# Kernel optimization log

Hardware: AMD Instinct MI355X
Metric: run time of the kernel (lower is better)

Reference implementation:

```python
import jax, jax.numpy as jnp
import numpy as np

D_MODEL = 1024
NUM_HEADS = 16
D_K = D_MODEL // NUM_HEADS
B, S = 2, 2048


def setup_inputs() -> dict:
    key = jax.random.key(0)
    ks = jax.random.split(key, 11)
    sc = 1.0 / np.sqrt(D_MODEL)
    return {
        "Q_input": jax.random.normal(ks[0], (B, S, D_MODEL), jnp.float32),
        "K_input": jax.random.normal(ks[1], (B, S, D_MODEL), jnp.float32),
        "V_input": jax.random.normal(ks[2], (B, S, D_MODEL), jnp.float32),
        "Wq": jax.random.normal(ks[3], (D_MODEL, D_MODEL), jnp.float32) * sc,
        "bq": jax.random.normal(ks[4], (D_MODEL,), jnp.float32) * 0.01,
        "Wk": jax.random.normal(ks[5], (D_MODEL, D_MODEL), jnp.float32) * sc,
        "bk": jax.random.normal(ks[6], (D_MODEL,), jnp.float32) * 0.01,
        "Wv": jax.random.normal(ks[7], (D_MODEL, D_MODEL), jnp.float32) * sc,
        "bv": jax.random.normal(ks[8], (D_MODEL,), jnp.float32) * 0.01,
        "Wo": jax.random.normal(ks[9], (D_MODEL, D_MODEL), jnp.float32) * sc,
        "bo": jax.random.normal(ks[10], (D_MODEL,), jnp.float32) * 0.01,
    }


def reference(Q_input, K_input, V_input, Wq, bq, Wk, bk, Wv, bv, Wo, bo):
    # Linear projections (torch Linear: x @ W.T + b)
    Q = Q_input @ Wq.T + bq  # [B,S,D]
    K = K_input @ Wk.T + bk
    V = V_input @ Wv.T + bv
    # split heads -> [B,H,S,dk]
    def split(x):
        return x.reshape(B, S, NUM_HEADS, D_K).transpose(0, 2, 1, 3)
    Qh, Kh, Vh = split(Q), split(K), split(V)
    scale = 1.0 / jnp.sqrt(jnp.asarray(D_K, Qh.dtype))
    scores = jnp.einsum('bhqd,bhkd->bhqk', Qh, Kh) * scale  # [B,H,S,S]
    attn = jax.nn.softmax(scores, axis=-1)
    ctx = jnp.einsum('bhqk,bhkd->bhqd', attn, Vh)  # [B,H,S,dk]
    concat = ctx.transpose(0, 2, 1, 3).reshape(B, S, D_MODEL)
    out = concat @ Wo.T + bo  # dropout is identity in eval
    return out
```

## Files before the change

### kernel.cpp

```cpp
#include <hip/hip_runtime.h>
#include <stdint.h>

#define DM   1024
#define NH   16
#define DKH  64
#define BBATCH 2
#define SEQ  2048
#define MTOK (BBATCH*SEQ)

typedef unsigned short u16;
typedef __attribute__((ext_vector_type(8))) short  bf16x8;
typedef __attribute__((ext_vector_type(4))) float  f32x4;

struct PtrArr11 { const void* p[11]; };
struct U16Arr11 { u16* p[11]; };

__device__ __forceinline__ float bf2f(u16 u) {
  union { unsigned int i; float f; } z; z.i = ((unsigned int)u) << 16; return z.f;
}
__device__ __forceinline__ u16 f2bf(float f) {
  union { float f; unsigned int i; } z; z.f = f;
  unsigned int i = z.i + 0x7fffu + ((z.i >> 16) & 1u);
  return (u16)(i >> 16);
}
__device__ __forceinline__ u16 f2bf_fast(float f) {
  union { float f; unsigned int i; } z; z.f = f;
  return (u16)((z.i + 0x8000u) >> 16);
}

__device__ __forceinline__ void gld16(const void* g, void* l) {
  __builtin_amdgcn_global_load_lds(
      (const __attribute__((address_space(1))) void*)g,
      (__attribute__((address_space(3))) void*)l,
      16, 0, 0);
}

__global__ void k_detect(const unsigned int* __restrict__ w, int* __restrict__ flag) {
  const int ln = threadIdx.x & 63;
  const unsigned int word = w[ln];
  const unsigned int ex = (word >> 7) & 0xFFu;
  const int hit = (ex >= 100u && ex <= 126u) ? 1 : 0;
  unsigned long long m = __ballot(hit);
  if (ln == 0) *flag = (__popcll(m) >= 40) ? 0 : 1;
}

__global__ __launch_bounds__(256) void k_convert_all(PtrArr11 src, U16Arr11 dst,
                                                     const int* __restrict__ flag) {
  if (*flag == 0) return;
  const int b = blockIdx.x;
  int seg, base;
  if      (b <  2048) { seg = 0;  base = 0;    }
  else if (b <  4096) { seg = 1;  base = 2048; }
  else if (b <  6144) { seg = 2;  base = 4096; }
  else if (b <  6656) { seg = 3;  base = 6144; }
  else if (b == 6656) { seg = 4;  base = 6656; }
  else if (b <  7169) { seg = 5;  base = 6657; }
  else if (b == 7169) { seg = 6;  base = 7169; }
  else if (b <  7682) { seg = 7;  base = 7170; }
  else if (b == 7682) { seg = 8;  base = 7682; }
  else if (b <  8195) { seg = 9;  base = 7683; }
  else                { seg = 10; base = 8195; }
  const int n = (seg < 3) ? (MTOK * DM) : ((seg & 1) ? (DM * DM) : DM);
  const int i0 = (b - base) * 2048 + threadIdx.x * 8;
  if (i0 >= n) return;
  const float* s = (const float*)src.p[seg] + i0;
  bf16x8 o;
#pragma unroll
  for (int j = 0; j < 8; ++j) o[j] = (short)f2bf(s[j]);
  *(bf16x8*)(dst.p[seg] + i0) = o;
}

__device__ __forceinline__ void gemm_body(const u16* __restrict__ X,
                                          const u16* __restrict__ W,
                                          const u16* __restrict__ bias,
                                          void* __restrict__ out,
                                          int isf32out)
{
  __shared__ __attribute__((aligned(16))) u16 sA[128 * 32];
  __shared__ __attribute__((aligned(16))) u16 sB[128 * 32];
  const int tid = threadIdx.x;
  const int ln = tid & 63, wv = tid >> 6;
  const int wm = wv & 1, wn = wv >> 1;
  const int m0 = blockIdx.y * 128, n0 = blockIdx.x * 128;
  const int fr = ln & 15, fq = ln >> 4;
  const int srow = ln >> 2, sslot = (ln & 3) * 8;

  f32x4 acc[4][4];
#pragma unroll
  for (int i = 0; i < 4; ++i)
#pragma unroll
    for (int j = 0; j < 4; ++j) acc[i][j] = (f32x4){0.f, 0.f, 0.f, 0.f};

  const u16* pA = X + (size_t)(m0 + wv * 32 + srow) * DM + sslot;
  const u16* pB = W + (size_t)(n0 + wv * 32 + srow) * DM + sslot;
  u16* lA0 = sA + (wv * 2) * 512; u16* lA1 = sA + (wv * 2 + 1) * 512;
  u16* lB0 = sB + (wv * 2) * 512; u16* lB1 = sB + (wv * 2 + 1) * 512;

  for (int k0 = 0; k0 < DM; k0 += 32) {
    gld16(pA + k0,            lA0);
    gld16(pA + 16 * DM + k0,  lA1);
    gld16(pB + k0,            lB0);
    gld16(pB + 16 * DM + k0,  lB1);
    asm volatile("s_waitcnt vmcnt(0)" ::: "memory");
    __syncthreads();

    bf16x8 af[4], bfg[4];
#pragma unroll
    for (int t = 0; t < 4; ++t) {
      af[t]  = *(const bf16x8*)(sA + (wm * 64 + t * 16 + fr) * 32 + fq * 8);
      bfg[t] = *(const bf16x8*)(sB + (wn * 64 + t * 16 + fr) * 32 + fq * 8);
    }
#pragma unroll
    for (int i = 0; i < 4; ++i)
#pragma unroll
      for (int j = 0; j < 4; ++j)
        acc[i][j] = __builtin_amdgcn_mfma_f32_16x16x32_bf16(af[i], bfg[j], acc[i][j], 0, 0, 0);
    __syncthreads();
  }

#pragma unroll
  for (int i = 0; i < 4; ++i) {
    const int row = m0 + wm * 64 + i * 16 + fq * 4;
#pragma unroll
    for (int j = 0; j < 4; ++j) {
      const int col = n0 + wn * 64 + j * 16 + fr;
      const float bv = bf2f(bias[col]);
#pragma unroll
      for (int r = 0; r < 4; ++r) {
        const float val = acc[i][j][r] + bv;
        const size_t idx = (size_t)(row + r) * DM + col;
        if (isf32out) ((float*)out)[idx] = val;
        else          ((u16*)out)[idx]   = f2bf(val);
      }
    }
  }
}

__global__ __launch_bounds__(256, 2) void k_gemm_qkv(
    PtrArr11 orig, U16Arr11 conv, const int* __restrict__ flag,
    u16* oq, u16* ok, u16* ov)
{
  const int f = *flag;
  const int z = blockIdx.z;
  const u16* X  = f ? conv.p[z]         : (const u16*)orig.p[z];
  const u16* W  = f ? conv.p[3 + 2 * z] : (const u16*)orig.p[3 + 2 * z];
  const u16* bi = f ? conv.p[4 + 2 * z] : (const u16*)orig.p[4 + 2 * z];
  u16* o = (z == 0) ? oq : (z == 1) ? ok : ov;
  gemm_body(X, W, bi, o, 0);
}

__global__ __launch_bounds__(256, 2) void k_gemm_one(
    const u16* X, const void* Wo_o, const u16* Wo_c,
    const void* bo_o, const u16* bo_c, const int* __restrict__ flag, void* o)
{
  const int f = *flag;
  const u16* W  = f ? Wo_c : (const u16*)Wo_o;
  const u16* bi = f ? bo_c : (const u16*)bo_o;
  gemm_body(X, W, bi, o, f);
}

__global__ __launch_bounds__(256) void k_transpose(const u16* __restrict__ in,
                                                   u16* __restrict__ out)
{
  __shared__ u16 t[64][66];
  const int b = blockIdx.z;
  const int s0 = blockIdx.x * 64, d0 = blockIdx.y * 64;
  const int c = threadIdx.x & 63, r0 = threadIdx.x >> 6;
#pragma unroll
  for (int i = 0; i < 16; ++i) {
    const int r = r0 + 4 * i;
    t[r][c] = in[(size_t)(b * SEQ + s0 + r) * DM + d0 + c];
  }
  __syncthreads();
#pragma unroll
  for (int i = 0; i < 16; ++i) {
    const int r = r0 + 4 * i;
    out[(size_t)(b * DM + d0 + r) * SEQ + s0 + c] = t[c][r];
  }
}

__global__ __launch_bounds__(256, 4) void k_attn(
    const u16* __restrict__ Qp, const u16* __restrict__ Kp,
    const u16* __restrict__ Vt, u16* __restrict__ ctx)
{
  __shared__ __attribute__((aligned(16))) u16 sK[64 * 72];
  __shared__ __attribute__((aligned(16))) u16 sV[64 * 72];
  __shared__ __attribute__((aligned(16))) u16 sP[4][16 * 72];

  const int tid = threadIdx.x;
  const int ln = tid & 63, wv = tid >> 6;
  const int bh = blockIdx.y;
  const int b = bh >> 4, h = bh & 15;
  const int q0 = blockIdx.x * 64 + wv * 16;
  const int fr = ln & 15, fq = ln >> 4;
  const int str = tid >> 2, stq = (tid & 3) * 16;

  bf16x8 qf[2];
#pragma unroll
  for (int ks = 0; ks < 2; ++ks) {
    const u16* src = Qp + (size_t)(b * SEQ + q0 + fr) * DM + h * DKH + ks * 32 + fq * 8;
    bf16x8 v = *(const bf16x8*)src;
    bf16x8 w;
#pragma unroll
    for (int j = 0; j < 8; ++j)
      w[j] = (short)f2bf(bf2f((u16)v[j]) * 0.125f);
    qf[ks] = w;
  }

  float l_acc[4] = {0.f, 0.f, 0.f, 0.f};
  f32x4 o_acc[4];
#pragma unroll
  for (int dt = 0; dt < 4; ++dt) o_acc[dt] = (f32x4){0.f, 0.f, 0.f, 0.f};

  u16* myP = sP[wv];

  for (int kb = 0; kb < SEQ / 64; ++kb) {
    const int key0 = kb * 64;
    {
      const u16* gK = Kp + (size_t)(b * SEQ + key0 + str) * DM + h * DKH + stq;
      const u16* gV = Vt + (size_t)(b * DM + h * DKH + str) * SEQ + key0 + stq;
      *(bf16x8*)(sK + str * 72 + stq)     = *(const bf16x8*)gK;
      *(bf16x8*)(sK + str * 72 + stq + 8) = *(const bf16x8*)(gK + 8);
      *(bf16x8*)(sV + str * 72 + stq)     = *(const bf16x8*)gV;
      *(bf16x8*)(sV + str * 72 + stq + 8) = *(const bf16x8*)(gV + 8);
    }
    __syncthreads();

    bf16x8 kf[4][2];
#pragma unroll
    for (int nt = 0; nt < 4; ++nt)
#pragma unroll
      for (int ks = 0; ks < 2; ++ks)
        kf[nt][ks] = *(const bf16x8*)(sK + (nt * 16 + fr) * 72 + ks * 32 + fq * 8);

    f32x4 s_acc[4];
#pragma unroll
    for (int nt = 0; nt < 4; ++nt) s_acc[nt] = (f32x4){0.f, 0.f, 0.f, 0.f};
#pragma unroll
    for (int nt = 0; nt < 4; ++nt)
#pragma unroll
      for (int ks = 0; ks < 2; ++ks)
        s_acc[nt] = __builtin_amdgcn_mfma_f32_16x16x32_bf16(qf[ks], kf[nt][ks], s_acc[nt], 0, 0, 0);

#pragma unroll
    for (int nt = 0; nt < 4; ++nt)
#pragma unroll
      for (int r = 0; r < 4; ++r) {
        const float p = __expf(s_acc[nt][r]);
        l_acc[r] += p;
        myP[(fq * 4 + r) * 72 + nt * 16 + fr] = f2bf_fast(p);
      }
    asm volatile("s_waitcnt lgkmcnt(0)" ::: "memory");

    bf16x8 pf[2], vf[4][2];
#pragma unroll
    for (int ks = 0; ks < 2; ++ks)
      pf[ks] = *(const bf16x8*)(myP + fr * 72 + ks * 32 + fq * 8);
#pragma unroll
    for (int dt = 0; dt < 4; ++dt)
#pragma unroll
      for (int ks = 0; ks < 2; ++ks)
        vf[dt][ks] = *(const bf16x8*)(sV + (dt * 16 + fr) * 72 + ks * 32 + fq * 8);
#pragma unroll
    for (int dt = 0; dt < 4; ++dt)
#pragma unroll
      for (int ks = 0; ks < 2; ++ks)
        o_acc[dt] = __builtin_amdgcn_mfma_f32_16x16x32_bf16(pf[ks], vf[dt][ks], o_acc[dt], 0, 0, 0);

    __syncthreads();
  }

  float inv[4];
#pragma unroll
  for (int r = 0; r < 4; ++r) {
    float l = l_acc[r];
    l += __shfl_xor(l, 1);
    l += __shfl_xor(l, 2);
    l += __shfl_xor(l, 4);
    l += __shfl_xor(l, 8);
    inv[r] = 1.0f / l;
  }
#pragma unroll
  for (int dt = 0; dt < 4; ++dt)
#pragma unroll
    for (int r = 0; r < 4; ++r) {
      const int qrow = q0 + fq * 4 + r;
      const int col = h * DKH + dt * 16 + fr;
      ctx[(size_t)(b * SEQ + qrow) * DM + col] = f2bf(o_acc[dt][r] * inv[r]);
    }
}

extern "C" void kernel_launch(void* const* d_in, const int* in_sizes, int n_in,
                              void* d_out, int out_size, void* d_ws, size_t ws_size,
                              hipStream_t stream)
{
  char* ws = (char*)d_ws;
  int* flag = (int*)ws;

  const size_t TOKSZ = (size_t)MTOK * DM * sizeof(u16);
  const size_t WSZ   = (size_t)DM * DM * sizeof(u16);
  const size_t BSZ   = 4096;

  size_t off = 256;
  u16* Qc  = (u16*)(ws + off); off += TOKSZ;
  u16* Kc  = (u16*)(ws + off); off += TOKSZ;
  u16* Vc  = (u16*)(ws + off); off += TOKSZ;
  u16* Wqc = (u16*)(ws + off); off += WSZ;
  u16* Wkc = (u16*)(ws + off); off += WSZ;
  u16* Wvc = (u16*)(ws + off); off += WSZ;
  u16* Woc = (u16*)(ws + off); off += WSZ;
  u16* bqc = (u16*)(ws + off); off += BSZ;
  u16* bkc = (u16*)(ws + off); off += BSZ;
  u16* bvc = (u16*)(ws + off); off += BSZ;
  u16* boc = (u16*)(ws + off); off += BSZ;
  u16* Qp  = (u16*)(ws + off); off += TOKSZ;
  u16* Kp  = (u16*)(ws + off); off += TOKSZ;
  u16* Vp  = (u16*)(ws + off); off += TOKSZ;
  u16* Vt  = Qc;
  u16* ctx = Kc;

  PtrArr11 orig;
  for (int i = 0; i < 11; ++i) orig.p[i] = d_in[i];
  U16Arr11 conv;
  conv.p[0] = Qc;  conv.p[1] = Kc;  conv.p[2] = Vc;
  conv.p[3] = Wqc; conv.p[4] = bqc; conv.p[5] = Wkc; conv.p[6] = bkc;
  conv.p[7] = Wvc; conv.p[8] = bvc; conv.p[9] = Woc; conv.p[10] = boc;

  dim3 blk(256);

  k_detect<<<1, 64, 0, stream>>>((const unsigned int*)d_in[3], flag);
  k_convert_all<<<8196, blk, 0, stream>>>(orig, conv, flag);
  k_gemm_qkv<<<dim3(DM / 128, MTOK / 128, 3), blk, 0, stream>>>(
      orig, conv, flag, Qp, Kp, Vp);
  k_transpose<<<dim3(SEQ / 64, DM / 64, BBATCH), blk, 0, stream>>>(Vp, Vt);
  k_attn<<<dim3(SEQ / 64, BBATCH * NH), blk, 0, stream>>>(Qp, Kp, Vt, ctx);
  k_gemm_one<<<dim3(DM / 128, MTOK / 128, 1), blk, 0, stream>>>(
      ctx, d_in[9], Woc, d_in[10], boc, flag, d_out);
}
```

Before: 260.0 us.

## Compute transposed scores, keep P in registers via bpermute, double query rows per wave

The attention kernel now computes S^T = K·Q^T, so probabilities come out laid out per query column. They are packed to bf16 pairs and rearranged into the MFMA B-operand with ds_bpermute, which removes the LDS round-trip for P and its waitcnt. Each wave now handles 32 query rows (two m-tiles) against each staged K/V tile, halving the grid and doubling K/V reuse from LDS. The costs are higher register pressure (launch bounds lowered from 4 to 2) and fewer blocks in flight.

```diff
diff --git a/kernel.cpp b/kernel.cpp
--- a/kernel.cpp
+++ b/kernel.cpp
@@ -23,9 +23,9 @@
   unsigned int i = z.i + 0x7fffu + ((z.i >> 16) & 1u);
   return (u16)(i >> 16);
 }
-__device__ __forceinline__ u16 f2bf_fast(float f) {
-  union { float f; unsigned int i; } z; z.f = f;
-  return (u16)((z.i + 0x8000u) >> 16);
+__device__ __forceinline__ unsigned pack2bf(float lo, float hi) {
+  union { float f; unsigned int i; } a, b; a.f = lo; b.f = hi;
+  return ((a.i + 0x8000u) >> 16) | (((b.i + 0x8000u) >> 16) << 16);
 }
 
 __device__ __forceinline__ void gld16(const void* g, void* l) {
@@ -179,40 +179,44 @@
   }
 }
 
-__global__ __launch_bounds__(256, 4) void k_attn(
+__global__ __launch_bounds__(256, 2) void k_attn(
     const u16* __restrict__ Qp, const u16* __restrict__ Kp,
     const u16* __restrict__ Vt, u16* __restrict__ ctx)
 {
   __shared__ __attribute__((aligned(16))) u16 sK[64 * 72];
   __shared__ __attribute__((aligned(16))) u16 sV[64 * 72];
-  __shared__ __attribute__((aligned(16))) u16 sP[4][16 * 72];
 
   const int tid = threadIdx.x;
   const int ln = tid & 63, wv = tid >> 6;
   const int bh = blockIdx.y;
   const int b = bh >> 4, h = bh & 15;
-  const int q0 = blockIdx.x * 64 + wv * 16;
+  const int q0 = blockIdx.x * 128 + wv * 32;
   const int fr = ln & 15, fq = ln >> 4;
   const int str = tid >> 2, stq = (tid & 3) * 16;
 
-  bf16x8 qf[2];
-#pragma unroll
-  for (int ks = 0; ks < 2; ++ks) {
-    const u16* src = Qp + (size_t)(b * SEQ + q0 + fr) * DM + h * DKH + ks * 32 + fq * 8;
-    bf16x8 v = *(const bf16x8*)src;
-    bf16x8 w;
-#pragma unroll
-    for (int j = 0; j < 8; ++j)
-      w[j] = (short)f2bf(bf2f((u16)v[j]) * 0.125f);
-    qf[ks] = w;
-  }
-
-  float l_acc[4] = {0.f, 0.f, 0.f, 0.f};
-  f32x4 o_acc[4];
-#pragma unroll
-  for (int dt = 0; dt < 4; ++dt) o_acc[dt] = (f32x4){0.f, 0.f, 0.f, 0.f};
-
-  u16* myP = sP[wv];
+  const int addr0 = 4 * (fr + 16 * ((fq & 1) * 2));
+  const int addr1 = addr0 + 64;
+
+  bf16x8 qf[2][2];
+#pragma unroll
+  for (int mt = 0; mt < 2; ++mt)
+#pragma unroll
+    for (int ks = 0; ks < 2; ++ks) {
+      const u16* src = Qp + (size_t)(b * SEQ + q0 + mt * 16 + fr) * DM + h * DKH + ks * 32 + fq * 8;
+      bf16x8 v = *(const bf16x8*)src;
+      bf16x8 w;
+#pragma unroll
+      for (int j = 0; j < 8; ++j)
+        w[j] = (short)f2bf(bf2f((u16)v[j]) * 0.125f);
+      qf[mt][ks] = w;
+    }
+
+  float l_acc[2] = {0.f, 0.f};
+  f32x4 o_acc[2][4];
+#pragma unroll
+  for (int mt = 0; mt < 2; ++mt)
+#pragma unroll
+    for (int dt = 0; dt < 4; ++dt) o_acc[mt][dt] = (f32x4){0.f, 0.f, 0.f, 0.f};
 
   for (int kb = 0; kb < SEQ / 64; ++kb) {
     const int key0 = kb * 64;
@@ -228,66 +232,83 @@
 
     bf16x8 kf[4][2];
 #pragma unroll
-    for (int nt = 0; nt < 4; ++nt)
+    for (int kt = 0; kt < 4; ++kt)
 #pragma unroll
       for (int ks = 0; ks < 2; ++ks)
-        kf[nt][ks] = *(const bf16x8*)(sK + (nt * 16 + fr) * 72 + ks * 32 + fq * 8);
-
-    f32x4 s_acc[4];
-#pragma unroll
-    for (int nt = 0; nt < 4; ++nt) s_acc[nt] = (f32x4){0.f, 0.f, 0.f, 0.f};
-#pragma unroll
-    for (int nt = 0; nt < 4; ++nt)
-#pragma unroll
-      for (int ks = 0; ks < 2; ++ks)
-        s_acc[nt] = __builtin_amdgcn_mfma_f32_16x16x32_bf16(qf[ks], kf[nt][ks], s_acc[nt], 0, 0, 0);
-
-#pragma unroll
-    for (int nt = 0; nt < 4; ++nt)
-#pragma unroll
-      for (int r = 0; r < 4; ++r) {
-        const float p = __expf(s_acc[nt][r]);
-        l_acc[r] += p;
-        myP[(fq * 4 + r) * 72 + nt * 16 + fr] = f2bf_fast(p);
-      }
-    asm volatile("s_waitcnt lgkmcnt(0)" ::: "memory");
-
-    bf16x8 pf[2], vf[4][2];
-#pragma unroll
-    for (int ks = 0; ks < 2; ++ks)
-      pf[ks] = *(const bf16x8*)(myP + fr * 72 + ks * 32 + fq * 8);
+        kf[kt][ks] = *(const bf16x8*)(sK + (kt * 16 + fr) * 72 + ks * 32 + fq * 8);
+
+    bf16x8 vf[4][2];
 #pragma unroll
     for (int dt = 0; dt < 4; ++dt)
 #pragma unroll
       for (int ks = 0; ks < 2; ++ks)
         vf[dt][ks] = *(const bf16x8*)(sV + (dt * 16 + fr) * 72 + ks * 32 + fq * 8);
+
+#pragma unroll
+    for (int mt = 0; mt < 2; ++mt) {
+      f32x4 s2[4];
+#pragma unroll
+      for (int kt = 0; kt < 4; ++kt) s2[kt] = (f32x4){0.f, 0.f, 0.f, 0.f};
+#pragma unroll
+      for (int kt = 0; kt < 4; ++kt)
+#pragma unroll
+        for (int ks = 0; ks < 2; ++ks)
+          s2[kt] = __builtin_amdgcn_mfma_f32_16x16x32_bf16(kf[kt][ks], qf[mt][ks], s2[kt], 0, 0, 0);
+
+      unsigned pk[4][2];
+#pragma unroll
+      for (int kt = 0; kt < 4; ++kt) {
+        float p0 = __expf(s2[kt][0]), p1 = __expf(s2[kt][1]);
+        float p2 = __expf(s2[kt][2]), p3 = __expf(s2[kt][3]);
+        l_acc[mt] += (p0 + p1) + (p2 + p3);
+        pk[kt][0] = pack2bf(p0, p1);
+        pk[kt][1] = pack2bf(p2, p3);
+      }
+
+      bf16x8 pb[2];
+#pragma unroll
+      for (int ks = 0; ks < 2; ++ks) {
+        union { unsigned u[4]; bf16x8 v; } cv;
+#pragma unroll
+        for (int pp = 0; pp < 4; ++pp) {
+          const int addr = (pp >> 1) ? addr1 : addr0;
+          const int vlo = __builtin_amdgcn_ds_bpermute(addr, (int)pk[ks * 2][pp & 1]);
+          const int vhi = __builtin_amdgcn_ds_bpermute(addr, (int)pk[ks * 2 + 1][pp & 1]);
+          cv.u[pp] = (fq >= 2) ? (unsigned)vhi : (unsigned)vlo;
+        }
+        pb[ks] = cv.v;
+      }
+
+#pragma unroll
+      for (int dt = 0; dt < 4; ++dt)
+#pragma unroll
+        for (int ks = 0; ks < 2; ++ks)
+          o_acc[mt][dt] = __builtin_amdgcn_mfma_f32_16x16x32_bf16(vf[dt][ks], pb[ks], o_acc[mt][dt], 0, 0, 0);
+    }
+
+    __syncthreads();
+  }
+
+  float inv[2];
+#pragma unroll
+  for (int mt = 0; mt < 2; ++mt) {
+    float l = l_acc[mt];
+    l += __shfl_xor(l, 16);
+    l += __shfl_xor(l, 32);
+    inv[mt] = 1.0f / l;
+  }
+
+#pragma unroll
+  for (int mt = 0; mt < 2; ++mt) {
+    const int qrow = q0 + mt * 16 + fr;
 #pragma unroll
     for (int dt = 0; dt < 4; ++dt)
 #pragma unroll
-      for (int ks = 0; ks < 2; ++ks)
-        o_acc[dt] = __builtin_amdgcn_mfma_f32_16x16x32_bf16(pf[ks], vf[dt][ks], o_acc[dt], 0, 0, 0);
-
-    __syncthreads();
-  }
-
-  float inv[4];
-#pragma unroll
-  for (int r = 0; r < 4; ++r) {
-    float l = l_acc[r];
-    l += __shfl_xor(l, 1);
-    l += __shfl_xor(l, 2);
-    l += __shfl_xor(l, 4);
-    l += __shfl_xor(l, 8);
-    inv[r] = 1.0f / l;
-  }
-#pragma unroll
-  for (int dt = 0; dt < 4; ++dt)
-#pragma unroll
-    for (int r = 0; r < 4; ++r) {
-      const int qrow = q0 + fq * 4 + r;
-      const int col = h * DKH + dt * 16 + fr;
-      ctx[(size_t)(b * SEQ + qrow) * DM + col] = f2bf(o_acc[dt][r] * inv[r]);
-    }
+      for (int r = 0; r < 4; ++r) {
+        const int col = h * DKH + dt * 16 + fq * 4 + r;
+        ctx[(size_t)(b * SEQ + qrow) * DM + col] = f2bf(o_acc[mt][dt][r] * inv[mt]);
+      }
+  }
 }
 
 extern "C" void kernel_launch(void* const* d_in, const int* in_sizes, int n_in,
@@ -333,7 +354,7 @@
   k_gemm_qkv<<<dim3(DM / 128, MTOK / 128, 3), blk, 0, stream>>>(
       orig, conv, flag, Qp, Kp, Vp);
   k_transpose<<<dim3(SEQ / 64, DM / 64, BBATCH), blk, 0, stream>>>(Vp, Vt);
-  k_attn<<<dim3(SEQ / 64, BBATCH * NH), blk, 0, stream>>>(Qp, Kp, Vt, ctx);
+  k_attn<<<dim3(SEQ / 128, BBATCH * NH), blk, 0, stream>>>(Qp, Kp, Vt, ctx);
   k_gemm_one<<<dim3(DM / 128, MTOK / 128, 1), blk, 0, stream>>>(
       ctx, d_in[9], Woc, d_in[10], boc, flag, d_out);
 }
```

Measured after the change: 260.5 us. About the same (+0.2%).
